# Performance work log

Hardware: AMD Instinct MI355X
Metric: run time of the kernel (lower is better)

The kernel has to match this reference:

```python
import jax, jax.numpy as jnp
import numpy as np

B, N, D = 1, 1024, 3584
H, KVH, HD = 28, 4, 128
I = 18944
SEC = [16, 24, 24]  # mrope_section, sums to HD//2
EPS_RMS = 1e-6
EPS_SM = 1e-6


def setup_inputs() -> dict:
    key = jax.random.key(0)
    ks = jax.random.split(key, 16)
    s = 0.02
    return {
        "hidden_states": jax.random.normal(ks[0], (B, N, D), jnp.float32),
        "cos": jax.random.uniform(ks[1], (3, B, N, HD), jnp.float32, -1.0, 1.0),
        "sin": jax.random.uniform(ks[2], (3, B, N, HD), jnp.float32, -1.0, 1.0),
        "prune_mask": jax.random.randint(ks[3], (B, N), 0, 2, jnp.int32),
        "Wq": jax.random.normal(ks[4], (D, H * HD), jnp.float32) * s,
        "bq": jnp.zeros((H * HD,), jnp.float32),
        "Wk": jax.random.normal(ks[5], (D, KVH * HD), jnp.float32) * s,
        "bk": jnp.zeros((KVH * HD,), jnp.float32),
        "Wv": jax.random.normal(ks[6], (D, KVH * HD), jnp.float32) * s,
        "bv": jnp.zeros((KVH * HD,), jnp.float32),
        "Wo": jax.random.normal(ks[7], (H * HD, D), jnp.float32) * s,
        "ln1_w": jnp.ones((D,), jnp.float32),
        "ln2_w": jnp.ones((D,), jnp.float32),
        "Wg": jax.random.normal(ks[8], (D, I), jnp.float32) * s,
        "Wu": jax.random.normal(ks[9], (D, I), jnp.float32) * s,
        "Wd": jax.random.normal(ks[10], (I, D), jnp.float32) * s,
    }


def _rmsnorm(x, w):
    v = jnp.mean(x * x, axis=-1, keepdims=True)
    return x * jax.lax.rsqrt(v + EPS_RMS) * w


def _rotate_half(x):
    h = x.shape[-1] // 2
    return jnp.concatenate([-x[..., h:], x[..., :h]], axis=-1)


def _mrope_select(t):
    # t: (3, B, N, HD) -> (B, 1, N, HD), picking section i from axis i%3
    parts, idx = [], 0
    for i, s in enumerate(SEC * 2):
        parts.append(t[i % 3, :, :, idx:idx + s])
        idx += s
    return jnp.concatenate(parts, axis=-1)[:, None]


def reference(hidden_states, cos, sin, prune_mask, Wq, bq, Wk, bk, Wv, bv, Wo,
              ln1_w, ln2_w, Wg, Wu, Wd):
    x = _rmsnorm(hidden_states, ln1_w)
    q = (x @ Wq + bq).reshape(B, N, H, HD).transpose(0, 2, 1, 3)
    k = (x @ Wk + bk).reshape(B, N, KVH, HD).transpose(0, 2, 1, 3)
    v = (x @ Wv + bv).reshape(B, N, KVH, HD).transpose(0, 2, 1, 3)

    cf, sf = _mrope_select(cos), _mrope_select(sin)
    q = q * cf + _rotate_half(q) * sf
    k = k * cf + _rotate_half(k) * sf

    groups = H // KVH
    k = jnp.repeat(k, groups, axis=1)  # (B,H,N,HD)
    v = jnp.repeat(v, groups, axis=1)

    scores = jnp.einsum("bhqd,bhkd->bhqk", q, k) / np.sqrt(HD).astype(np.float32)
    causal = jnp.tril(jnp.ones((N, N), bool))
    scores = jnp.where(causal, scores, jnp.float32(-1e9))

    # custom prune-masked softmax (softmax_with_mask)
    am = prune_mask.astype(jnp.float32)[:, None, None, :]  # (B,1,1,N)
    eye = jnp.eye(N, dtype=jnp.float32)
    am = am + (1.0 - am) * eye
    mx = jnp.max(scores, axis=-1, keepdims=True)
    e = jnp.exp(scores - mx) * am
    attn = (e + EPS_SM / N) / (jnp.sum(e, axis=-1, keepdims=True) + EPS_SM)

    o = jnp.einsum("bhqk,bhkd->bhqd", attn, v)
    o = o.transpose(0, 2, 1, 3).reshape(B, N, H * HD) @ Wo

    h = hidden_states + o
    y = _rmsnorm(h, ln2_w)
    mlp = (jax.nn.silu(y @ Wg) * (y @ Wu)) @ Wd
    return h + mlp
```

## Files before the change

kernel.cpp:

```cpp
#include <hip/hip_runtime.h>
#include <hip/hip_bf16.h>


#define SEQ   1024
#define DIM   3584
#define NH    28
#define NKVH  4
#define HDIM  128
#define IDIM  18944
#define QKVN  4608
#define GUN   37888

typedef __attribute__((ext_vector_type(8))) __bf16 bf16x8;
typedef __attribute__((ext_vector_type(4))) __bf16 bf16x4;
typedef __attribute__((ext_vector_type(4))) float  f32x4;

static constexpr size_t OFF_WQKVT = 0;
static constexpr size_t OFF_WOT   = OFF_WQKVT + (size_t)QKVN*DIM*2;
static constexpr size_t OFF_WGUT  = OFF_WOT   + (size_t)DIM*DIM*2;
static constexpr size_t OFF_WDT   = OFF_WGUT  + (size_t)GUN*DIM*2;
static constexpr size_t OFF_XB    = OFF_WDT   + (size_t)DIM*IDIM*2;
static constexpr size_t OFF_QKV   = OFF_XB    + (size_t)SEQ*DIM*2;
static constexpr size_t OFF_VT    = OFF_QKV   + (size_t)SEQ*QKVN*2;
static constexpr size_t OFF_VSUMP = OFF_VT    + (size_t)NKVH*HDIM*SEQ*2;
static constexpr size_t OFF_VSUM  = OFF_VSUMP + 4*8*128*4;
static constexpr size_t OFF_BQKV  = OFF_VSUM  + 4*128*4;
static constexpr size_t OFF_OB    = OFF_BQKV  + (size_t)QKVN*4;
static constexpr size_t OFF_HB    = OFF_OB    + (size_t)SEQ*DIM*2;
static constexpr size_t OFF_YB    = OFF_HB    + (size_t)SEQ*DIM*4;
static constexpr size_t OFF_GU    = OFF_YB    + (size_t)SEQ*DIM*2;
static constexpr size_t OFF_PB    = OFF_GU    + (size_t)SEQ*GUN*2;
static constexpr size_t OFF_PART  = OFF_GU;

#define GLL16(gp, lp)                                                        \
  __builtin_amdgcn_global_load_lds(                                         \
      (const __attribute__((address_space(1))) void*)(gp),                  \
      (__attribute__((address_space(3))) void*)(lp), 16, 0, 0)

#define BAR    asm volatile("s_barrier" ::: "memory")

__global__ __launch_bounds__(256) void transconv_kernel(
    const float* __restrict__ W, __bf16* __restrict__ WT, int K, int N, int mode)
{
  __shared__ __bf16 t[64][72];
  const int tid = threadIdx.x;
  const int k0 = blockIdx.y * 64, n0 = blockIdx.x * 64;
#pragma unroll
  for (int it = 0; it < 4; ++it) {
    int idx = it * 256 + tid;
    int r = idx >> 4, c4 = idx & 15;
    float4 v = *(const float4*)(W + (size_t)(k0 + r) * N + n0 + c4 * 4);
    t[r][c4 * 4 + 0] = (__bf16)v.x;
    t[r][c4 * 4 + 1] = (__bf16)v.y;
    t[r][c4 * 4 + 2] = (__bf16)v.z;
    t[r][c4 * 4 + 3] = (__bf16)v.w;
  }
  __syncthreads();
#pragma unroll
  for (int it = 0; it < 2; ++it) {
    int idx = it * 256 + tid;
    int r = idx >> 3, c8 = idx & 7;
    bf16x8 o;
#pragma unroll
    for (int i = 0; i < 8; ++i) o[i] = t[c8 * 8 + i][r];
    const int nlog = n0 + r;
    const int orow = (mode == 0) ? nlog
                   : ((nlog >> 4) << 5) + ((mode == 2) ? 16 : 0) + (nlog & 15);
    *(bf16x8*)(WT + (size_t)orow * K + k0 + c8 * 8) = o;
  }
}

__global__ __launch_bounds__(256) void pack_bias_kernel(
    const float* __restrict__ bq, const float* __restrict__ bk,
    const float* __restrict__ bv, float* __restrict__ out)
{
  int i = blockIdx.x * 256 + threadIdx.x;
  if (i < DIM) out[i] = bq[i];
  else if (i < DIM + 512) out[i] = bk[i - DIM];
  else if (i < QKVN) out[i] = bv[i - DIM - 512];
}

__global__ __launch_bounds__(256) void rmsnorm_kernel(
    const float* __restrict__ in, const float* __restrict__ w,
    __bf16* __restrict__ out)
{
  const int row = blockIdx.x;
  const int t = threadIdx.x;
  const float* x = in + (size_t)row * DIM;
  float4 v[4];
  float ss = 0.f;
#pragma unroll
  for (int i = 0; i < 4; ++i) {
    int idx = t + i * 256;
    if (idx < 896) {
      v[i] = ((const float4*)x)[idx];
      ss += v[i].x * v[i].x + v[i].y * v[i].y + v[i].z * v[i].z + v[i].w * v[i].w;
    }
  }
#pragma unroll
  for (int m = 1; m < 64; m <<= 1) ss += __shfl_xor(ss, m);
  __shared__ float red[4];
  if ((t & 63) == 0) red[t >> 6] = ss;
  __syncthreads();
  float tot = red[0] + red[1] + red[2] + red[3];
  float rs = rsqrtf(tot / (float)DIM + 1e-6f);
#pragma unroll
  for (int i = 0; i < 4; ++i) {
    int idx = t + i * 256;
    if (idx < 896) {
      float4 wv = ((const float4*)w)[idx];
      bf16x4 o;
      o[0] = (__bf16)(v[i].x * rs * wv.x);
      o[1] = (__bf16)(v[i].y * rs * wv.y);
      o[2] = (__bf16)(v[i].z * rs * wv.z);
      o[3] = (__bf16)(v[i].w * rs * wv.w);
      *(bf16x4*)(out + (size_t)row * DIM + idx * 4) = o;
    }
  }
}

__global__ __launch_bounds__(256, 2) void gemm_splitk_kernel(
    const __bf16* __restrict__ A, const __bf16* __restrict__ BT,
    float* __restrict__ PART, int M, int N, int K, int Kc, int gridY)
{
  __shared__ __bf16 As[128 * 64];
  __shared__ __bf16 Bs[128 * 64];
  const int tid = threadIdx.x;
  const int l = tid & 63, w = tid >> 6;

  const int nwg = gridDim.x;
  const int bq8 = nwg >> 3, br8 = nwg & 7;
  const int xcd = blockIdx.x & 7, bidx = blockIdx.x >> 3;
  const int wg = (xcd < br8 ? xcd * (bq8 + 1) : br8 * (bq8 + 1) + (xcd - br8) * bq8) + bidx;
  const int tm = wg % gridY;
  const int wg2 = wg / gridY;
  const int gridX = N >> 7;
  const int tn = wg2 % gridX;
  const int ks = wg2 / gridX;
  const int row0 = tm * 128;
  const int col0 = tn * 128;
  const int kbase = ks * Kc;

  const int m0 = (w >> 1) * 64;
  const int n0 = (w & 1) * 64;
  const int lg = l >> 4, lc = l & 15;

  f32x4 acc[4][4] = {};

  size_t aoff[4], boff[4];
  int lbyte[4];
#pragma unroll
  for (int it = 0; it < 4; ++it) {
    const int cbase = (it * 4 + w) * 64;
    const int c = cbase + l;
    const int r = c >> 3, p = c & 7;
    const int b = p ^ (r & 7);
    aoff[it] = (size_t)(row0 + r) * K + kbase + b * 8;
    boff[it] = (size_t)(col0 + r) * K + kbase + b * 8;
    lbyte[it] = cbase * 16;
  }
  const int sw = lc & 7;

  const int ktc = Kc >> 6;
  for (int kt = 0; kt < ktc; ++kt) {
    const int k0 = kt << 6;
#pragma unroll
    for (int it = 0; it < 4; ++it) {
      GLL16(A + aoff[it] + k0, (char*)As + lbyte[it]);
      GLL16(BT + boff[it] + k0, (char*)Bs + lbyte[it]);
    }
    __syncthreads();
#pragma unroll
    for (int s = 0; s < 2; ++s) {
      bf16x8 af[4], bfv[4];
#pragma unroll
      for (int a = 0; a < 4; ++a)
        af[a] = *(const bf16x8*)(As + (m0 + a * 16 + lc) * 64 + ((s * 4 + lg) ^ sw) * 8);
#pragma unroll
      for (int b = 0; b < 4; ++b)
        bfv[b] = *(const bf16x8*)(Bs + (n0 + b * 16 + lc) * 64 + ((s * 4 + lg) ^ sw) * 8);
#pragma unroll
      for (int a = 0; a < 4; ++a)
#pragma unroll
        for (int b = 0; b < 4; ++b)
          acc[a][b] = __builtin_amdgcn_mfma_f32_16x16x32_bf16(af[a], bfv[b], acc[a][b], 0, 0, 0);
    }
    __syncthreads();
  }

  float* P = PART + (size_t)ks * M * N;
  const int lr = lg * 4;
#pragma unroll
  for (int b = 0; b < 4; ++b) {
    const int col = col0 + n0 + b * 16 + lc;
#pragma unroll
    for (int a = 0; a < 4; ++a)
#pragma unroll
      for (int j = 0; j < 4; ++j)
        P[(size_t)(row0 + m0 + a * 16 + lr + j) * N + col] = acc[a][b][j];
  }
}

template<int S, bool BF16OUT, bool BIAS>
__global__ __launch_bounds__(256) void reduce_kernel(
    const float* __restrict__ part, const float* __restrict__ resid,
    const float* __restrict__ bias, void* __restrict__ out, int N, int MN4)
{
  const int i4 = blockIdx.x * 256 + threadIdx.x;
  if (i4 >= MN4) return;
  const size_t base = (size_t)i4 * 4;
  f32x4 s = *(const f32x4*)(part + base);
#pragma unroll
  for (int k = 1; k < S; ++k)
    s += *(const f32x4*)(part + (size_t)k * MN4 * 4 + base);
  if (BIAS) {
    const int col = (int)(base % N);
    s += *(const f32x4*)(bias + col);
  }
  if (resid != nullptr) s += *(const f32x4*)(resid + base);
  if (BF16OUT) {
    bf16x4 o;
#pragma unroll
    for (int j = 0; j < 4; ++j) o[j] = (__bf16)s[j];
    *(bf16x4*)((__bf16*)out + base) = o;
  } else {
    *(f32x4*)((float*)out + base) = s;
  }
}

template<int EPI>
__global__ __launch_bounds__(512, 1) void gemm256_kernel(
    const __bf16* __restrict__ A, const __bf16* __restrict__ BT,
    void* __restrict__ OUT, int M, int N, int K, int Kc, int gridY)
{
  __shared__ int4 lds4[8192];
  char* ldsc = (char*)lds4;
  const int tid = threadIdx.x;
  const int l = tid & 63, w = tid >> 6;
  const int wr = w >> 2, wc = w & 3;
  const int lg = l >> 4, lc = l & 15;

  const int nwg = gridDim.x;
  const int bq8 = nwg >> 3, br8 = nwg & 7;
  const int xcd = blockIdx.x & 7, bidx = blockIdx.x >> 3;
  const int wg = (xcd < br8 ? xcd * (bq8 + 1) : br8 * (bq8 + 1) + (xcd - br8) * bq8) + bidx;
  const int ntn = N >> 8;
  const int wg2 = wg / gridY;
  const int row0 = (wg % gridY) * 256;
  const int col0 = (wg2 % ntn) * 256;
  const int ks = wg2 / ntn;
  const int kbase = ks * Kc;

  size_t aoffj[2], boffj[2];
  int dstj[2];
#pragma unroll
  for (int j = 0; j < 2; ++j) {
    const int c = (j * 8 + w) * 64 + l;
    const int r = c >> 3, p = c & 7;
    const int b = p ^ (r & 7);
    aoffj[j] = (size_t)(row0 + r) * K + kbase + b * 8;
    boffj[j] = (size_t)(col0 + r) * K + kbase + b * 8;
    dstj[j] = (j * 8 + w) * 1024;
  }

#define STG_A(U, KT, BUFB) do {                                              \
    GLL16(A + aoffj[0] + (size_t)(U) * 128 * K + (size_t)(KT) * 64,          \
          ldsc + (BUFB) + (U) * 16384 + dstj[0]);                            \
    GLL16(A + aoffj[1] + (size_t)(U) * 128 * K + (size_t)(KT) * 64,          \
          ldsc + (BUFB) + (U) * 16384 + dstj[1]); } while (0)
#define STG_B(U, KT, BUFB) do {                                              \
    GLL16(BT + boffj[0] + (size_t)(U) * 128 * K + (size_t)(KT) * 64,         \
          ldsc + (BUFB) + 32768 + (U) * 16384 + dstj[0]);                    \
    GLL16(BT + boffj[1] + (size_t)(U) * 128 * K + (size_t)(KT) * 64,         \
          ldsc + (BUFB) + 32768 + (U) * 16384 + dstj[1]); } while (0)

  const int sw = lc & 7;
  const int rdA = (wr * 128 + lc) * 128;
  const int rdB = 32768 + (wc * 64 + lc) * 128;
  const int sk0 = (lg ^ sw) * 16;
  const int sk1 = ((4 | lg) ^ sw) * 16;

  f32x4 acc[8][4] = {};
  bf16x8 af[4][2], bfr[4][2];

#define RD_A4(MH, BUFB) do { _Pragma("unroll")                               \
    for (int mm = 0; mm < 4; ++mm) {                                         \
      af[mm][0] = *(const bf16x8*)(ldsc + (BUFB) + rdA + ((MH) * 4 + mm) * 2048 + sk0); \
      af[mm][1] = *(const bf16x8*)(ldsc + (BUFB) + rdA + ((MH) * 4 + mm) * 2048 + sk1); } } while (0)
#define RD_B2(NL, BUFB) do { _Pragma("unroll")                               \
    for (int nn = 0; nn < 2; ++nn) {                                         \
      bfr[(NL) + nn][0] = *(const bf16x8*)(ldsc + (BUFB) + rdB + ((NL) + nn) * 2048 + sk0); \
      bfr[(NL) + nn][1] = *(const bf16x8*)(ldsc + (BUFB) + rdB + ((NL) + nn) * 2048 + sk1); } } while (0)

#define MFMA16(MH, NL) do { _Pragma("unroll")                                \
    for (int mm = 0; mm < 4; ++mm) { _Pragma("unroll")                       \
      for (int nn = 0; nn < 2; ++nn) {                                       \
        acc[(MH)*4+mm][(NL)+nn] = __builtin_amdgcn_mfma_f32_16x16x32_bf16(   \
            af[mm][0], bfr[(NL)+nn][0], acc[(MH)*4+mm][(NL)+nn], 0, 0, 0);   \
        acc[(MH)*4+mm][(NL)+nn] = __builtin_amdgcn_mfma_f32_16x16x32_bf16(   \
            af[mm][1], bfr[(NL)+nn][1], acc[(MH)*4+mm][(NL)+nn], 0, 0, 0); } } } while (0)

#define KTILE(BUFB, TNEXT)                                                   \
    RD_A4(0, BUFB); RD_B2(0, BUFB);                                          \
    __builtin_amdgcn_s_setprio(1); MFMA16(0, 0);                             \
    __builtin_amdgcn_s_setprio(0);                                           \
    RD_B2(2, BUFB);                                                          \
    __builtin_amdgcn_s_setprio(1); MFMA16(0, 2);                             \
    __builtin_amdgcn_s_setprio(0);                                           \
    RD_A4(1, BUFB);                                                          \
    __builtin_amdgcn_s_setprio(1); MFMA16(1, 2);                             \
    __builtin_amdgcn_s_setprio(0);                                           \
    asm volatile("s_waitcnt lgkmcnt(0)" ::: "memory");                       \
    BAR;                                    \
    STG_A(0, TNEXT, BUFB); STG_A(1, TNEXT, BUFB);                            \
    STG_B(0, TNEXT, BUFB); STG_B(1, TNEXT, BUFB);                            \
    __builtin_amdgcn_s_setprio(1); MFMA16(1, 0);                             \
    __builtin_amdgcn_s_setprio(0);                                           \
    asm volatile("s_waitcnt vmcnt(8)" ::: "memory");  \
    BAR

  STG_A(0, 0, 0); STG_A(1, 0, 0); STG_B(0, 0, 0); STG_B(1, 0, 0);
  STG_A(0, 1, 65536); STG_A(1, 1, 65536); STG_B(0, 1, 65536); STG_B(1, 1, 65536);
  asm volatile("s_waitcnt vmcnt(8)" ::: "memory");
  BAR;

  const int T = Kc >> 6;
#pragma unroll 1
  for (int i = 0; i < (T >> 1); ++i) {
    const int t0 = 2 * i;
    const int se = (t0 + 2 < T) ? t0 + 2 : 0;
    const int so = (t0 + 3 < T) ? t0 + 3 : 0;
    KTILE(0, se);
    KTILE(65536, so);
  }
  asm volatile("s_waitcnt vmcnt(0)" ::: "memory");

  if (EPI == 0) {
    __bf16* PBo = (__bf16*)OUT;
    const int id = N >> 1;
    const int baseq = (col0 + wc * 64) >> 5;
#pragma unroll
    for (int m = 0; m < 8; ++m) {
#pragma unroll
      for (int p = 0; p < 2; ++p) {
        const int gcol = (baseq + p) * 16 + lc;
#pragma unroll
        for (int j = 0; j < 4; ++j) {
          const int row = row0 + wr * 128 + m * 16 + lg * 4 + j;
          const float g = acc[m][2 * p][j];
          const float u = acc[m][2 * p + 1][j];
          const float s = g / (1.f + __expf(-g));
          PBo[(size_t)row * id + gcol] = (__bf16)(s * u);
        }
      }
    }
  } else {
    float* P = (float*)OUT + (size_t)ks * M * N;
#pragma unroll
    for (int m = 0; m < 8; ++m)
#pragma unroll
      for (int n = 0; n < 4; ++n)
#pragma unroll
        for (int j = 0; j < 4; ++j)
          P[(size_t)(row0 + wr * 128 + m * 16 + lg * 4 + j) * N
            + (col0 + wc * 64 + n * 16 + lc)] = acc[m][n][j];
  }
#undef STG_A
#undef STG_B
#undef RD_A4
#undef RD_B2
#undef MFMA16
#undef KTILE
}

__global__ __launch_bounds__(256) void rope_kernel(
    __bf16* __restrict__ qkv, const float* __restrict__ cosb,
    const float* __restrict__ sinb)
{
  const int n = blockIdx.x;
  for (int p = threadIdx.x; p < 32 * 64; p += 256) {
    const int head = p >> 6;
    const int d = p & 63;
    const int src = (d < 16) ? 0 : (d < 40) ? 1 : 2;
    const float* cb = cosb + (size_t)src * SEQ * HDIM + (size_t)n * HDIM;
    const float* sb = sinb + (size_t)src * SEQ * HDIM + (size_t)n * HDIM;
    const float c0 = cb[d], c1 = cb[d + 64];
    const float s0 = sb[d], s1 = sb[d + 64];
    const int col = (head < NH) ? head * HDIM : DIM + (head - NH) * HDIM;
    __bf16* q = qkv + (size_t)n * QKVN + col;
    const float a = (float)q[d];
    const float b = (float)q[d + 64];
    q[d]      = (__bf16)(a * c0 - b * s0);
    q[d + 64] = (__bf16)(b * c1 + a * s1);
  }
}

__global__ __launch_bounds__(256) void vtrans_kernel(
    const __bf16* __restrict__ qkv, __bf16* __restrict__ vT,
    float* __restrict__ vsump)
{
  __shared__ __bf16 t[128][132];
  const int nt = blockIdx.x, kvh = blockIdx.y;
  const int n0 = nt * 128;
  const int tid = threadIdx.x;
#pragma unroll
  for (int it = 0; it < 8; ++it) {
    int idx = it * 256 + tid;
    int nl = idx >> 4, c8 = idx & 15;
    bf16x8 v = *(const bf16x8*)(qkv + (size_t)(n0 + nl) * QKVN + 4096 + kvh * HDIM + c8 * 8);
#pragma unroll
    for (int i = 0; i < 8; ++i) t[nl][c8 * 8 + i] = v[i];
  }
  __syncthreads();
#pragma unroll
  for (int it = 0; it < 8; ++it) {
    int idx = it * 256 + tid;
    int d = idx >> 4, c8 = idx & 15;
    bf16x8 o;
#pragma unroll
    for (int i = 0; i < 8; ++i) o[i] = t[c8 * 8 + i][d];
    *(bf16x8*)(vT + (size_t)(kvh * HDIM + d) * SEQ + n0 + c8 * 8) = o;
  }
  if (tid < 128) {
    float s = 0.f;
    for (int nl = 0; nl < 128; ++nl) s += (float)t[nl][tid];
    vsump[(size_t)(kvh * 8 + nt) * 128 + tid] = s;
  }
}

__global__ __launch_bounds__(512) void vsum_reduce_kernel(
    const float* __restrict__ vsump, float* __restrict__ vsum)
{
  const int idx = threadIdx.x;
  const int kvh = idx >> 7, d = idx & 127;
  float s = 0.f;
#pragma unroll
  for (int nt = 0; nt < 8; ++nt) s += vsump[(size_t)(kvh * 8 + nt) * 128 + d];
  vsum[idx] = s;
}

__global__ __launch_bounds__(256) void attn_kernel(
    const __bf16* __restrict__ qkv, const __bf16* __restrict__ vT,
    const float* __restrict__ vsum, const int* __restrict__ prune,
    __bf16* __restrict__ o)
{
  __shared__ __bf16 plds[4 * 16 * 40];
  const int tid = threadIdx.x;
  const int l = tid & 63, w = tid >> 6;
  const int h = blockIdx.y;
  const int kvh = h / 7;
  const int qt = blockIdx.x;
  const int qbase = qt * 64 + w * 16;
  const int lg = l >> 4, lc = l & 15;
  __bf16* pw = plds + w * (16 * 40);

  bf16x8 qf[4];
#pragma unroll
  for (int s = 0; s < 4; ++s)
    qf[s] = *(const bf16x8*)(qkv + (size_t)(qbase + lc) * QKVN + h * HDIM + s * 32 + lg * 8);

  f32x4 oacc[8] = {};
  float mrun[4] = {-3e38f, -3e38f, -3e38f, -3e38f};
  float lrun[4] = {0.f, 0.f, 0.f, 0.f};

  const int kbEnd = ((qbase + 15) >> 5) + 1;
  for (int kb = 0; kb < kbEnd; ++kb) {
    f32x4 sacc[2] = {};
#pragma unroll
    for (int s = 0; s < 4; ++s) {
#pragma unroll
      for (int c = 0; c < 2; ++c) {
        bf16x8 kf = *(const bf16x8*)(qkv + (size_t)(kb * 32 + c * 16 + lc) * QKVN
                                     + DIM + kvh * HDIM + s * 32 + lg * 8);
        sacc[c] = __builtin_amdgcn_mfma_f32_16x16x32_bf16(qf[s], kf, sacc[c], 0, 0, 0);
      }
    }
    float p[2][4];
    int am[2];
#pragma unroll
    for (int c = 0; c < 2; ++c) {
      const int col = kb * 32 + c * 16 + lc;
      am[c] = (prune[col] != 0) ? 1 : 0;
#pragma unroll
      for (int j = 0; j < 4; ++j) {
        const int row = qbase + lg * 4 + j;
        float sv = sacc[c][j] * 0.08838834764831845f;
        p[c][j] = (col <= row) ? sv : -3e38f;
      }
    }
#pragma unroll
    for (int j = 0; j < 4; ++j) {
      float mx = fmaxf(p[0][j], p[1][j]);
      mx = fmaxf(mx, __shfl_xor(mx, 1));
      mx = fmaxf(mx, __shfl_xor(mx, 2));
      mx = fmaxf(mx, __shfl_xor(mx, 4));
      mx = fmaxf(mx, __shfl_xor(mx, 8));
      const float mnew = fmaxf(mrun[j], mx);
      const float scale = __expf(mrun[j] - mnew);
      mrun[j] = mnew;
      const int row = qbase + lg * 4 + j;
      float rs = 0.f;
#pragma unroll
      for (int c = 0; c < 2; ++c) {
        const int col = kb * 32 + c * 16 + lc;
        float e = __expf(p[c][j] - mnew);
        const int keep = (col == row) ? 1 : am[c];
        e = keep ? e : 0.f;
        p[c][j] = e;
        rs += e;
      }
      rs += __shfl_xor(rs, 1);
      rs += __shfl_xor(rs, 2);
      rs += __shfl_xor(rs, 4);
      rs += __shfl_xor(rs, 8);
      lrun[j] = lrun[j] * scale + rs;
#pragma unroll
      for (int df = 0; df < 8; ++df) oacc[df][j] *= scale;
    }
#pragma unroll
    for (int c = 0; c < 2; ++c)
#pragma unroll
      for (int j = 0; j < 4; ++j)
        pw[(lg * 4 + j) * 40 + c * 16 + lc] = (__bf16)p[c][j];
    bf16x8 pa = *(const bf16x8*)(pw + lc * 40 + lg * 8);
#pragma unroll
    for (int df = 0; df < 8; ++df) {
      bf16x8 vf = *(const bf16x8*)(vT + (size_t)(kvh * HDIM + df * 16 + lc) * SEQ + kb * 32 + lg * 8);
      oacc[df] = __builtin_amdgcn_mfma_f32_16x16x32_bf16(pa, vf, oacc[df], 0, 0, 0);
    }
  }
#pragma unroll
  for (int df = 0; df < 8; ++df) {
    const float vs = vsum[kvh * HDIM + df * 16 + lc];
#pragma unroll
    for (int j = 0; j < 4; ++j) {
      const int row = qbase + lg * 4 + j;
      const float denom = lrun[j] + 1e-6f;
      const float val = (oacc[df][j] + 9.765625e-10f * vs) / denom;
      o[(size_t)row * DIM + h * HDIM + df * 16 + lc] = (__bf16)val;
    }
  }
}

extern "C" void kernel_launch(void* const* d_in, const int* in_sizes, int n_in,
                              void* d_out, int out_size, void* d_ws, size_t ws_size,
                              hipStream_t stream) {
  const float* hidden = (const float*)d_in[0];
  const float* cosb   = (const float*)d_in[1];
  const float* sinb   = (const float*)d_in[2];
  const int*   prune  = (const int*)d_in[3];
  const float* Wq     = (const float*)d_in[4];
  const float* bq     = (const float*)d_in[5];
  const float* Wk     = (const float*)d_in[6];
  const float* bk     = (const float*)d_in[7];
  const float* Wv     = (const float*)d_in[8];
  const float* bv     = (const float*)d_in[9];
  const float* Wo     = (const float*)d_in[10];
  const float* ln1    = (const float*)d_in[11];
  const float* ln2    = (const float*)d_in[12];
  const float* Wg     = (const float*)d_in[13];
  const float* Wu     = (const float*)d_in[14];
  const float* Wd     = (const float*)d_in[15];
  float* out = (float*)d_out;
  char* ws = (char*)d_ws;

  __bf16* WQKVT = (__bf16*)(ws + OFF_WQKVT);
  __bf16* WOT   = (__bf16*)(ws + OFF_WOT);
  __bf16* WGUT  = (__bf16*)(ws + OFF_WGUT);
  __bf16* WDT   = (__bf16*)(ws + OFF_WDT);
  __bf16* XB    = (__bf16*)(ws + OFF_XB);
  __bf16* QKV   = (__bf16*)(ws + OFF_QKV);
  __bf16* VT    = (__bf16*)(ws + OFF_VT);
  float*  VSUMP = (float*)(ws + OFF_VSUMP);
  float*  VSUM  = (float*)(ws + OFF_VSUM);
  float*  BQKV  = (float*)(ws + OFF_BQKV);
  __bf16* OB    = (__bf16*)(ws + OFF_OB);
  float*  HB    = (float*)(ws + OFF_HB);
  __bf16* YB    = (__bf16*)(ws + OFF_YB);
  __bf16* PB    = (__bf16*)(ws + OFF_PB);
  float*  PART  = (float*)(ws + OFF_PART);

  transconv_kernel<<<dim3(DIM / 64, DIM / 64), 256, 0, stream>>>(Wq, WQKVT, DIM, DIM, 0);
  transconv_kernel<<<dim3(512 / 64, DIM / 64), 256, 0, stream>>>(Wk, WQKVT + (size_t)DIM * DIM, DIM, 512, 0);
  transconv_kernel<<<dim3(512 / 64, DIM / 64), 256, 0, stream>>>(Wv, WQKVT + (size_t)4096 * DIM, DIM, 512, 0);
  pack_bias_kernel<<<QKVN / 256, 256, 0, stream>>>(bq, bk, bv, BQKV);
  rmsnorm_kernel<<<SEQ, 256, 0, stream>>>(hidden, ln1, XB);

  gemm_splitk_kernel<<<(QKVN / 128) * (SEQ / 128) * 2, 256, 0, stream>>>(
      XB, WQKVT, PART, SEQ, QKVN, DIM, DIM / 2, SEQ / 128);
  reduce_kernel<2, true, true><<<(SEQ * QKVN / 4 + 255) / 256, 256, 0, stream>>>(
      PART, nullptr, BQKV, QKV, QKVN, SEQ * QKVN / 4);

  rope_kernel<<<SEQ, 256, 0, stream>>>(QKV, cosb, sinb);
  vtrans_kernel<<<dim3(8, NKVH), 256, 0, stream>>>(QKV, VT, VSUMP);
  vsum_reduce_kernel<<<1, 512, 0, stream>>>(VSUMP, VSUM);
  attn_kernel<<<dim3(SEQ / 64, NH), 256, 0, stream>>>(QKV, VT, VSUM, prune, OB);

  transconv_kernel<<<dim3(DIM / 64, DIM / 64), 256, 0, stream>>>(Wo, WOT, DIM, DIM, 0);
  gemm256_kernel<1><<<(DIM / 256) * (SEQ / 256) * 4, 512, 0, stream>>>(
      OB, WOT, PART, SEQ, DIM, DIM, DIM / 4, SEQ / 256);
  reduce_kernel<4, false, false><<<(SEQ * DIM / 4 + 255) / 256, 256, 0, stream>>>(
      PART, hidden, nullptr, HB, DIM, SEQ * DIM / 4);

  rmsnorm_kernel<<<SEQ, 256, 0, stream>>>(HB, ln2, YB);

  transconv_kernel<<<dim3(IDIM / 64, DIM / 64), 256, 0, stream>>>(Wg, WGUT, DIM, IDIM, 1);
  transconv_kernel<<<dim3(IDIM / 64, DIM / 64), 256, 0, stream>>>(Wu, WGUT, DIM, IDIM, 2);
  gemm256_kernel<0><<<(GUN / 256) * (SEQ / 256), 512, 0, stream>>>(
      YB, WGUT, PB, SEQ, GUN, DIM, DIM, SEQ / 256);

  transconv_kernel<<<dim3(DIM / 64, IDIM / 64), 256, 0, stream>>>(Wd, WDT, IDIM, DIM, 0);
  gemm256_kernel<1><<<(DIM / 256) * (SEQ / 256) * 4, 512, 0, stream>>>(
      PB, WDT, PART, SEQ, DIM, IDIM, IDIM / 4, SEQ / 256);
  reduce_kernel<4, false, false><<<(SEQ * DIM / 4 + 255) / 256, 256, 0, stream>>>(
      PART, HB, nullptr, out, DIM, SEQ * DIM / 4);
}
```

Before: 972.8 us.

## Rework gemm256 main loop into finer interleaved pipeline and use it for QKV

Restructures the gemm256 double-buffered K loop so each quarter of MFMA work is interleaved with partial global-to-LDS stages for the next tile, separated by barriers and targeted waitcnts (vmcnt(4), lgkmcnt(0)). The QKV projection now uses gemm256 (256x256 tiles, 512 threads, split-K 2) instead of the separate 128x128 split-K kernel, which is deleted. The aim is better overlap of loads with MFMA and more reuse per tile. The trade-off is many more barriers per iteration and fewer workgroups for the QKV GEMM (144 vs 576), which could reduce occupancy.

```diff
diff --git a/kernel.cpp b/kernel.cpp
--- a/kernel.cpp
+++ b/kernel.cpp
@@ -38,6 +38,8 @@
       (__attribute__((address_space(3))) void*)(lp), 16, 0, 0)
 
 #define BAR    asm volatile("s_barrier" ::: "memory")
+#define LGKM0  asm volatile("s_waitcnt lgkmcnt(0)" ::: "memory")
+#define VM4    asm volatile("s_waitcnt vmcnt(4)" ::: "memory")
 
 __global__ __launch_bounds__(256) void transconv_kernel(
     const float* __restrict__ W, __bf16* __restrict__ WT, int K, int N, int mode)
@@ -119,88 +121,6 @@
   }
 }
 
-__global__ __launch_bounds__(256, 2) void gemm_splitk_kernel(
-    const __bf16* __restrict__ A, const __bf16* __restrict__ BT,
-    float* __restrict__ PART, int M, int N, int K, int Kc, int gridY)
-{
-  __shared__ __bf16 As[128 * 64];
-  __shared__ __bf16 Bs[128 * 64];
-  const int tid = threadIdx.x;
-  const int l = tid & 63, w = tid >> 6;
-
-  const int nwg = gridDim.x;
-  const int bq8 = nwg >> 3, br8 = nwg & 7;
-  const int xcd = blockIdx.x & 7, bidx = blockIdx.x >> 3;
-  const int wg = (xcd < br8 ? xcd * (bq8 + 1) : br8 * (bq8 + 1) + (xcd - br8) * bq8) + bidx;
-  const int tm = wg % gridY;
-  const int wg2 = wg / gridY;
-  const int gridX = N >> 7;
-  const int tn = wg2 % gridX;
-  const int ks = wg2 / gridX;
-  const int row0 = tm * 128;
-  const int col0 = tn * 128;
-  const int kbase = ks * Kc;
-
-  const int m0 = (w >> 1) * 64;
-  const int n0 = (w & 1) * 64;
-  const int lg = l >> 4, lc = l & 15;
-
-  f32x4 acc[4][4] = {};
-
-  size_t aoff[4], boff[4];
-  int lbyte[4];
-#pragma unroll
-  for (int it = 0; it < 4; ++it) {
-    const int cbase = (it * 4 + w) * 64;
-    const int c = cbase + l;
-    const int r = c >> 3, p = c & 7;
-    const int b = p ^ (r & 7);
-    aoff[it] = (size_t)(row0 + r) * K + kbase + b * 8;
-    boff[it] = (size_t)(col0 + r) * K + kbase + b * 8;
-    lbyte[it] = cbase * 16;
-  }
-  const int sw = lc & 7;
-
-  const int ktc = Kc >> 6;
-  for (int kt = 0; kt < ktc; ++kt) {
-    const int k0 = kt << 6;
-#pragma unroll
-    for (int it = 0; it < 4; ++it) {
-      GLL16(A + aoff[it] + k0, (char*)As + lbyte[it]);
-      GLL16(BT + boff[it] + k0, (char*)Bs + lbyte[it]);
-    }
-    __syncthreads();
-#pragma unroll
-    for (int s = 0; s < 2; ++s) {
-      bf16x8 af[4], bfv[4];
-#pragma unroll
-      for (int a = 0; a < 4; ++a)
-        af[a] = *(const bf16x8*)(As + (m0 + a * 16 + lc) * 64 + ((s * 4 + lg) ^ sw) * 8);
-#pragma unroll
-      for (int b = 0; b < 4; ++b)
-        bfv[b] = *(const bf16x8*)(Bs + (n0 + b * 16 + lc) * 64 + ((s * 4 + lg) ^ sw) * 8);
-#pragma unroll
-      for (int a = 0; a < 4; ++a)
-#pragma unroll
-        for (int b = 0; b < 4; ++b)
-          acc[a][b] = __builtin_amdgcn_mfma_f32_16x16x32_bf16(af[a], bfv[b], acc[a][b], 0, 0, 0);
-    }
-    __syncthreads();
-  }
-
-  float* P = PART + (size_t)ks * M * N;
-  const int lr = lg * 4;
-#pragma unroll
-  for (int b = 0; b < 4; ++b) {
-    const int col = col0 + n0 + b * 16 + lc;
-#pragma unroll
-    for (int a = 0; a < 4; ++a)
-#pragma unroll
-      for (int j = 0; j < 4; ++j)
-        P[(size_t)(row0 + m0 + a * 16 + lr + j) * N + col] = acc[a][b][j];
-  }
-}
-
 template<int S, bool BF16OUT, bool BIAS>
 __global__ __launch_bounds__(256) void reduce_kernel(
     const float* __restrict__ part, const float* __restrict__ resid,
@@ -300,38 +220,39 @@
         acc[(MH)*4+mm][(NL)+nn] = __builtin_amdgcn_mfma_f32_16x16x32_bf16(   \
             af[mm][1], bfr[(NL)+nn][1], acc[(MH)*4+mm][(NL)+nn], 0, 0, 0); } } } while (0)
 
-#define KTILE(BUFB, TNEXT)                                                   \
-    RD_A4(0, BUFB); RD_B2(0, BUFB);                                          \
-    __builtin_amdgcn_s_setprio(1); MFMA16(0, 0);                             \
-    __builtin_amdgcn_s_setprio(0);                                           \
-    RD_B2(2, BUFB);                                                          \
-    __builtin_amdgcn_s_setprio(1); MFMA16(0, 2);                             \
-    __builtin_amdgcn_s_setprio(0);                                           \
-    RD_A4(1, BUFB);                                                          \
-    __builtin_amdgcn_s_setprio(1); MFMA16(1, 2);                             \
-    __builtin_amdgcn_s_setprio(0);                                           \
-    asm volatile("s_waitcnt lgkmcnt(0)" ::: "memory");                       \
-    BAR;                                    \
-    STG_A(0, TNEXT, BUFB); STG_A(1, TNEXT, BUFB);                            \
-    STG_B(0, TNEXT, BUFB); STG_B(1, TNEXT, BUFB);                            \
-    __builtin_amdgcn_s_setprio(1); MFMA16(1, 0);                             \
-    __builtin_amdgcn_s_setprio(0);                                           \
-    asm volatile("s_waitcnt vmcnt(8)" ::: "memory");  \
-    BAR
-
-  STG_A(0, 0, 0); STG_A(1, 0, 0); STG_B(0, 0, 0); STG_B(1, 0, 0);
-  STG_A(0, 1, 65536); STG_A(1, 1, 65536); STG_B(0, 1, 65536); STG_B(1, 1, 65536);
-  asm volatile("s_waitcnt vmcnt(8)" ::: "memory");
+#define DO_MFMA(MH, NL)                                                      \
+    __builtin_amdgcn_s_setprio(1); MFMA16(MH, NL);                           \
+    __builtin_amdgcn_s_setprio(0)
+
+  STG_B(0, 0, 0); STG_B(1, 0, 0); STG_A(0, 0, 0); STG_A(1, 0, 0);
+  STG_B(0, 1, 65536); STG_B(1, 1, 65536);
+  VM4;
   BAR;
 
   const int T = Kc >> 6;
 #pragma unroll 1
   for (int i = 0; i < (T >> 1); ++i) {
-    const int t0 = 2 * i;
-    const int se = (t0 + 2 < T) ? t0 + 2 : 0;
-    const int so = (t0 + 3 < T) ? t0 + 3 : 0;
-    KTILE(0, se);
-    KTILE(65536, so);
+    const int t1 = 2 * i + 1;
+    const int se = (2 * i + 2 < T) ? 2 * i + 2 : 2 * i;
+    const int so = (2 * i + 3 < T) ? 2 * i + 3 : t1;
+    RD_A4(0, 0); RD_B2(0, 0); STG_A(0, t1, 65536);
+    BAR; LGKM0; DO_MFMA(0, 0); BAR;
+    RD_B2(2, 0); STG_A(1, t1, 65536);
+    BAR; LGKM0; DO_MFMA(0, 2); BAR;
+    RD_A4(1, 0); STG_B(0, se, 0);
+    BAR; LGKM0; DO_MFMA(1, 2); BAR;
+    STG_B(1, se, 0);
+    VM4;
+    BAR; DO_MFMA(1, 0); BAR;
+    RD_A4(0, 65536); RD_B2(0, 65536); STG_A(0, se, 0);
+    BAR; LGKM0; DO_MFMA(0, 0); BAR;
+    RD_B2(2, 65536); STG_A(1, se, 0);
+    BAR; LGKM0; DO_MFMA(0, 2); BAR;
+    RD_A4(1, 65536); STG_B(0, so, 65536);
+    BAR; LGKM0; DO_MFMA(1, 2); BAR;
+    STG_B(1, so, 65536);
+    VM4;
+    BAR; DO_MFMA(1, 0); BAR;
   }
   asm volatile("s_waitcnt vmcnt(0)" ::: "memory");
 
@@ -370,7 +291,7 @@
 #undef RD_A4
 #undef RD_B2
 #undef MFMA16
-#undef KTILE
+#undef DO_MFMA
 }
 
 __global__ __launch_bounds__(256) void rope_kernel(
@@ -586,8 +507,8 @@
   pack_bias_kernel<<<QKVN / 256, 256, 0, stream>>>(bq, bk, bv, BQKV);
   rmsnorm_kernel<<<SEQ, 256, 0, stream>>>(hidden, ln1, XB);
 
-  gemm_splitk_kernel<<<(QKVN / 128) * (SEQ / 128) * 2, 256, 0, stream>>>(
-      XB, WQKVT, PART, SEQ, QKVN, DIM, DIM / 2, SEQ / 128);
+  gemm256_kernel<1><<<(SEQ / 256) * (QKVN / 256) * 2, 512, 0, stream>>>(
+      XB, WQKVT, PART, SEQ, QKVN, DIM, DIM / 2, SEQ / 256);
   reduce_kernel<2, true, true><<<(SEQ * QKVN / 4 + 255) / 256, 256, 0, stream>>>(
       PART, nullptr, BQKV, QKV, QKVN, SEQ * QKVN / 4);
 
```

Measured after the change: 938.1 us. 3.6% less time.
